# Optimization experiments

Hardware: AMD Instinct MI355X
Metric: run time of the kernel (lower is better)

The kernel has to match this reference:

```python
import jax, jax.numpy as jnp
import numpy as np

B, S, H, F, V, MAX_OOV = 128, 512, 1024, 512, 50000, 50


def setup_inputs() -> dict:
    key = jax.random.key(0)
    ks = jax.random.split(key, 20)
    r = lambda i, shp, s=0.02: (jax.random.normal(ks[i], shp, jnp.float32) * s)
    return dict(
        input=jax.random.randint(ks[0], (B,), 0, V),
        hidden=jax.random.normal(ks[1], (1, B, H), jnp.float32) * 0.1,
        encoder_outputs=jax.random.normal(ks[2], (B, S, H), jnp.float32) * 0.1,
        x_padding_masks=jnp.ones((B, S), jnp.float32),
        len_oov=jax.random.randint(ks[3], (B,), 0, MAX_OOV),
        coverage_vector=jnp.zeros((B, S), jnp.float32),
        ref2tgt=jax.random.randint(ks[4], (B, S), 0, V + MAX_OOV),
        emb=r(5, (V, F)),
        W_ih=r(6, (3 * H, F)), W_hh=r(7, (3 * H, H)),
        b_ih=jnp.zeros(3 * H, jnp.float32), b_hh=jnp.zeros(3 * H, jnp.float32),
        e2v1_w=r(8, (F, H)), e2v1_b=jnp.zeros(F, jnp.float32),
        e2v2_w=r(9, (V, F)), e2v2_b=jnp.zeros(V, jnp.float32),
        fc_w=r(10, (H, 2 * H)), fc_b=jnp.zeros(H, jnp.float32),
        wgen_w=r(11, (1, 2 * H + F)), wgen_b=jnp.zeros(1, jnp.float32),
        att_Wh=r(12, (H, H)), att_Ws=r(13, (H, H)),
        att_wc=r(14, (H,)), att_b=jnp.zeros(H, jnp.float32), att_v=r(15, (H,)),
    )


def reference(input, hidden, encoder_outputs, x_padding_masks, len_oov,
              coverage_vector, ref2tgt, emb, W_ih, W_hh, b_ih, b_hh,
              e2v1_w, e2v1_b, e2v2_w, e2v2_b, fc_w, fc_b, wgen_w, wgen_b,
              att_Wh, att_Ws, att_wc, att_b, att_v):
    # embedding lookup (dropout is identity at inference)
    emb_x = emb[input]  # [B, F]

    # --- additive (Bahdanau) attention with coverage ---
    s = hidden[0]  # [B, H] (n_layers == 1)
    feat = jnp.tanh(
        jnp.einsum('bsh,kh->bsk', encoder_outputs, att_Wh)
        + (s @ att_Ws.T)[:, None, :]
        + coverage_vector[:, :, None] * att_wc
        + att_b)  # [B, S, H]
    e = jnp.einsum('bsh,h->bs', feat, att_v)  # [B, S]
    a = jax.nn.softmax(e, axis=1) * x_padding_masks
    a = a / (jnp.sum(a, axis=1, keepdims=True))  # [B, S] renormalized attn
    coverage_new = coverage_vector + a
    context = jnp.einsum('bs,bsh->bh', a, encoder_outputs)  # [B, H]
    h_att = jnp.concatenate([s, context], axis=-1) @ fc_w.T + fc_b  # [B, H]

    # --- single-step GRU (PyTorch gate order r, z, n) ---
    gi = emb_x @ W_ih.T + b_ih  # [B, 3H]
    gh = h_att @ W_hh.T + b_hh  # [B, 3H]
    i_r, i_z, i_n = jnp.split(gi, 3, axis=-1)
    h_r, h_z, h_n = jnp.split(gh, 3, axis=-1)
    r = jax.nn.sigmoid(i_r + h_r)
    z = jax.nn.sigmoid(i_z + h_z)
    n = jnp.tanh(i_n + r * h_n)
    h_new = (1.0 - z) * n + z * h_att  # [B, H]

    # --- vocab distribution ---
    out1 = h_new @ e2v1_w.T + e2v1_b  # [B, F]
    p_vocab = jax.nn.softmax(out1 @ e2v2_w.T + e2v2_b, axis=1)  # [B, V]

    # --- pointer-generator mixing ---
    x_gen = jnp.concatenate([context, h_new, emb_x], axis=-1)  # [B, 2H+F]
    p_gen = jax.nn.sigmoid(x_gen @ wgen_w.T + wgen_b)[:, 0]  # [B]
    p_gen = jnp.clip(p_gen, 0.001, 0.999)
    p_vocab_w = p_gen[:, None] * p_vocab  # [B, V]
    attn_w = (1.0 - p_gen)[:, None] * a  # [B, S]
    p_ext = jnp.concatenate([p_vocab_w, jnp.zeros((B, MAX_OOV), p_vocab_w.dtype)], axis=1)
    rows = jnp.arange(B)[:, None]
    final = p_ext.at[rows, ref2tgt].add(attn_w)  # scatter_add over extended vocab

    return final, h_new[None], coverage_new, a
```

## Files before the change

### kernel.cpp

```cpp
#include <hip/hip_runtime.h>
#include <math.h>

#define B_   128
#define S_   512
#define H_   1024
#define F_   512
#define V_   50000
#define OOV_ 50
#define EV_  (V_ + OOV_)

#define BM 128
#define BN 128
#define BK 64

typedef __attribute__((ext_vector_type(8))) __bf16 bf16x8;
typedef __attribute__((ext_vector_type(4))) __bf16 bf16x4;
typedef __attribute__((ext_vector_type(4))) float  f32x4;

__device__ __forceinline__ void gload_lds16(const void* g, void* lds) {
  __builtin_amdgcn_global_load_lds(
      (const __attribute__((address_space(1))) unsigned int*)g,
      (__attribute__((address_space(3))) unsigned int*)lds, 16, 0, 0);
}

__device__ __forceinline__ float fast_tanh(float x) {
  float v = fminf(fmaxf(x, -15.f), 15.f);
  float t = __expf(2.f * v);
  return 1.f - 2.f / (t + 1.f);
}

__global__ __launch_bounds__(256)
void cast_both_kernel(const float* __restrict__ enc, __bf16* __restrict__ enc_h,
                      const float* __restrict__ wh, __bf16* __restrict__ wh_h)
{
  const size_t n_enc = (size_t)B_ * S_ * H_;
  const size_t n_tot = n_enc + (size_t)H_ * H_;
  for (size_t i = ((size_t)blockIdx.x * 256 + threadIdx.x) * 8; i < n_tot;
       i += (size_t)gridDim.x * 256 * 8) {
    const float* in; __bf16* out; size_t j;
    if (i < n_enc) { in = enc; out = enc_h; j = i; }
    else           { in = wh;  out = wh_h;  j = i - n_enc; }
    float4 a = *(const float4*)(in + j);
    float4 b = *(const float4*)(in + j + 4);
    bf16x8 o;
    o[0] = (__bf16)a.x; o[1] = (__bf16)a.y; o[2] = (__bf16)a.z; o[3] = (__bf16)a.w;
    o[4] = (__bf16)b.x; o[5] = (__bf16)b.y; o[6] = (__bf16)b.z; o[7] = (__bf16)b.w;
    *(bf16x8*)(out + j) = o;
  }
}

__global__ __launch_bounds__(256)
void gemm_splitk(const float* __restrict__ A, const float* __restrict__ W,
                 float* __restrict__ partial, int N, int K, int KS)
{
  __shared__ float As[128 * 68];
  __shared__ float Ws[32 * 68];
  const int tid = threadIdx.x;
  const int n0 = blockIdx.x * 32;
  const int p  = blockIdx.y;
  const int tx = tid & 7, ty = tid >> 3;
  const int lr = tid >> 4, lc4 = (tid & 15) * 4;
  float acc[4][4] = {};
  const int kend = p * KS + KS;
  for (int k0 = p * KS; k0 < kend; k0 += 64) {
#pragma unroll
    for (int pp = 0; pp < 8; ++pp)
      *(float4*)(As + (pp * 16 + lr) * 68 + lc4) =
          *(const float4*)(A + (size_t)(pp * 16 + lr) * K + k0 + lc4);
#pragma unroll
    for (int pp = 0; pp < 2; ++pp)
      *(float4*)(Ws + (pp * 16 + lr) * 68 + lc4) =
          *(const float4*)(W + (size_t)(n0 + pp * 16 + lr) * K + k0 + lc4);
    __syncthreads();
#pragma unroll
    for (int kk = 0; kk < 16; ++kk) {
      float4 av[4], wv[4];
#pragma unroll
      for (int i = 0; i < 4; i++) av[i] = *(const float4*)(As + (ty * 4 + i) * 68 + kk * 4);
#pragma unroll
      for (int j = 0; j < 4; j++) wv[j] = *(const float4*)(Ws + (tx * 4 + j) * 68 + kk * 4);
#pragma unroll
      for (int i = 0; i < 4; i++)
#pragma unroll
        for (int j = 0; j < 4; j++) {
          acc[i][j] = fmaf(av[i].x, wv[j].x, acc[i][j]);
          acc[i][j] = fmaf(av[i].y, wv[j].y, acc[i][j]);
          acc[i][j] = fmaf(av[i].z, wv[j].z, acc[i][j]);
          acc[i][j] = fmaf(av[i].w, wv[j].w, acc[i][j]);
        }
    }
    __syncthreads();
  }
#pragma unroll
  for (int i = 0; i < 4; i++)
#pragma unroll
    for (int j = 0; j < 4; j++)
      partial[((size_t)p * 128 + ty * 4 + i) * N + n0 + tx * 4 + j] = acc[i][j];
}

__global__ __launch_bounds__(256)
void gemm_splitk_cat(const float* __restrict__ A1, const float* __restrict__ A2,
                     const float* __restrict__ W, float* __restrict__ partial,
                     int N, int K, int KS)
{
  __shared__ float As[128 * 68];
  __shared__ float Ws[32 * 68];
  const int tid = threadIdx.x;
  const int n0 = blockIdx.x * 32;
  const int p  = blockIdx.y;
  const int tx = tid & 7, ty = tid >> 3;
  const int lr = tid >> 4, lc4 = (tid & 15) * 4;
  const float* A = (p * KS < 1024) ? A1 : A2;
  const int kbase = (p * KS < 1024) ? 0 : 1024;
  float acc[4][4] = {};
  const int kend = p * KS + KS;
  for (int k0 = p * KS; k0 < kend; k0 += 64) {
#pragma unroll
    for (int pp = 0; pp < 8; ++pp)
      *(float4*)(As + (pp * 16 + lr) * 68 + lc4) =
          *(const float4*)(A + (size_t)(pp * 16 + lr) * 1024 + (k0 - kbase) + lc4);
#pragma unroll
    for (int pp = 0; pp < 2; ++pp)
      *(float4*)(Ws + (pp * 16 + lr) * 68 + lc4) =
          *(const float4*)(W + (size_t)(n0 + pp * 16 + lr) * K + k0 + lc4);
    __syncthreads();
#pragma unroll
    for (int kk = 0; kk < 16; ++kk) {
      float4 av[4], wv[4];
#pragma unroll
      for (int i = 0; i < 4; i++) av[i] = *(const float4*)(As + (ty * 4 + i) * 68 + kk * 4);
#pragma unroll
      for (int j = 0; j < 4; j++) wv[j] = *(const float4*)(Ws + (tx * 4 + j) * 68 + kk * 4);
#pragma unroll
      for (int i = 0; i < 4; i++)
#pragma unroll
        for (int j = 0; j < 4; j++) {
          acc[i][j] = fmaf(av[i].x, wv[j].x, acc[i][j]);
          acc[i][j] = fmaf(av[i].y, wv[j].y, acc[i][j]);
          acc[i][j] = fmaf(av[i].z, wv[j].z, acc[i][j]);
          acc[i][j] = fmaf(av[i].w, wv[j].w, acc[i][j]);
        }
    }
    __syncthreads();
  }
#pragma unroll
  for (int i = 0; i < 4; i++)
#pragma unroll
    for (int j = 0; j < 4; j++)
      partial[((size_t)p * 128 + ty * 4 + i) * N + n0 + tx * 4 + j] = acc[i][j];
}

__global__ __launch_bounds__(256)
void gemm_splitk_gather(const int* __restrict__ input, const float* __restrict__ emb,
                        const float* __restrict__ W, float* __restrict__ partial,
                        int N, int K, int KS)
{
  __shared__ float As[128 * 68];
  __shared__ float Ws[32 * 68];
  const int tid = threadIdx.x;
  const int n0 = blockIdx.x * 32;
  const int p  = blockIdx.y;
  const int tx = tid & 7, ty = tid >> 3;
  const int lr = tid >> 4, lc4 = (tid & 15) * 4;
  float acc[4][4] = {};
  const int kend = p * KS + KS;
  for (int k0 = p * KS; k0 < kend; k0 += 64) {
#pragma unroll
    for (int pp = 0; pp < 8; ++pp) {
      int row = input[pp * 16 + lr];
      *(float4*)(As + (pp * 16 + lr) * 68 + lc4) =
          *(const float4*)(emb + (size_t)row * K + k0 + lc4);
    }
#pragma unroll
    for (int pp = 0; pp < 2; ++pp)
      *(float4*)(Ws + (pp * 16 + lr) * 68 + lc4) =
          *(const float4*)(W + (size_t)(n0 + pp * 16 + lr) * K + k0 + lc4);
    __syncthreads();
#pragma unroll
    for (int kk = 0; kk < 16; ++kk) {
      float4 av[4], wv[4];
#pragma unroll
      for (int i = 0; i < 4; i++) av[i] = *(const float4*)(As + (ty * 4 + i) * 68 + kk * 4);
#pragma unroll
      for (int j = 0; j < 4; j++) wv[j] = *(const float4*)(Ws + (tx * 4 + j) * 68 + kk * 4);
#pragma unroll
      for (int i = 0; i < 4; i++)
#pragma unroll
        for (int j = 0; j < 4; j++) {
          acc[i][j] = fmaf(av[i].x, wv[j].x, acc[i][j]);
          acc[i][j] = fmaf(av[i].y, wv[j].y, acc[i][j]);
          acc[i][j] = fmaf(av[i].z, wv[j].z, acc[i][j]);
          acc[i][j] = fmaf(av[i].w, wv[j].w, acc[i][j]);
        }
    }
    __syncthreads();
  }
#pragma unroll
  for (int i = 0; i < 4; i++)
#pragma unroll
    for (int j = 0; j < 4; j++)
      partial[((size_t)p * 128 + ty * 4 + i) * N + n0 + tx * 4 + j] = acc[i][j];
}

__global__ __launch_bounds__(256)
void reduce_partial(const float* __restrict__ partial, const float* __restrict__ bias,
                    float* __restrict__ C, int N, int P)
{
  int idx = blockIdx.x * 256 + threadIdx.x;
  int n = idx % N;
  float s = bias ? bias[n] : 0.f;
  for (int p = 0; p < P; ++p) s += partial[(size_t)p * 128 * N + idx];
  C[idx] = s;
}

__global__ __launch_bounds__(256)
void reduce_partial_bf16(const float* __restrict__ partial, const float* __restrict__ bias,
                         __bf16* __restrict__ C, int N, int P)
{
  int idx = blockIdx.x * 256 + threadIdx.x;
  int n = idx % N;
  float s = bias ? bias[n] : 0.f;
  for (int p = 0; p < P; ++p) s += partial[(size_t)p * 128 * N + idx];
  C[idx] = (__bf16)s;
}

__global__ __launch_bounds__(512, 1)
void feat_mfma256_kernel(const __bf16* __restrict__ enc, const __bf16* __restrict__ Wh,
                         const float* __restrict__ pSWS, const float* __restrict__ cov,
                         const float* __restrict__ wcv, const float* __restrict__ ab,
                         const float* __restrict__ av_, float* __restrict__ e_part)
{
  __shared__ __attribute__((aligned(16))) __bf16 As[2][2][128 * 64];
  __shared__ __attribute__((aligned(16))) __bf16 Bs[2][2][128 * 64];
  const int tid  = threadIdx.x;
  const int lane = tid & 63, wid = tid >> 6;
  const int wr = wid >> 2, wc = wid & 3;
  const int bid = blockIdx.x;
  const int swz = (bid & 7) * 128 + (bid >> 3);
  const int mt = swz >> 2, nt = swz & 3;
  const int bs0 = mt * 256;
  const int n0  = nt * 256;
  const int b   = bs0 >> 9;

  const int scb = ((tid & 7) * 16) ^ (((tid >> 3) & 7) << 4);
  const __bf16* aS[2][2];
  const __bf16* bS[2][2];
#pragma unroll
  for (int h = 0; h < 2; ++h)
#pragma unroll
    for (int q = 0; q < 2; ++q) {
      int r = h * 128 + q * 64 + (tid >> 3);
      aS[h][q] = enc + (size_t)(bs0 + r) * H_ + (scb >> 1);
      bS[h][q] = Wh  + (size_t)(n0  + r) * H_ + (scb >> 1);
    }
  const int ldsQ0 = tid * 16, ldsQ1 = 8192 + tid * 16;

  const int lrow = lane & 15, kbase = (lane >> 4) << 4;
  const int bh = wc >> 1;
  int aO[8][2], bO[4][2];
#pragma unroll
  for (int m = 0; m < 8; ++m) {
    int rh = m * 16 + lrow, sw = (rh & 7) << 4;
    aO[m][0] = rh * 128 + (kbase ^ sw);
    aO[m][1] = rh * 128 + ((64 + kbase) ^ sw);
  }
#pragma unroll
  for (int n = 0; n < 4; ++n) {
    int rh = (wc & 1) * 64 + n * 16 + lrow, sw = (rh & 7) << 4;
    bO[n][0] = rh * 128 + (kbase ^ sw);
    bO[n][1] = rh * 128 + ((64 + kbase) ^ sw);
  }

  f32x4 acc[8][4];
#pragma unroll
  for (int i = 0; i < 8; i++)
#pragma unroll
    for (int j = 0; j < 4; j++) acc[i][j] = (f32x4){0.f, 0.f, 0.f, 0.f};
  bf16x8 bfv[4][2];

#define STG_A(d, h, ofs)                                                       \
  { gload_lds16(aS[h][0] + (ofs), (char*)As[d][h] + ldsQ0);                    \
    gload_lds16(aS[h][1] + (ofs), (char*)As[d][h] + ldsQ1); }
#define STG_B(d, h, ofs)                                                       \
  { gload_lds16(bS[h][0] + (ofs), (char*)Bs[d][h] + ldsQ0);                    \
    gload_lds16(bS[h][1] + (ofs), (char*)Bs[d][h] + ldsQ1); }
#define BAR()                                                                  \
  { __builtin_amdgcn_sched_barrier(0); __builtin_amdgcn_s_barrier();           \
    __builtin_amdgcn_sched_barrier(0); }
#define LGKM0()                                                                \
  { asm volatile("s_waitcnt lgkmcnt(0)" ::: "memory");                         \
    __builtin_amdgcn_sched_barrier(0); }
#define VMC(n)                                                                 \
  { asm volatile("s_waitcnt vmcnt(" #n ")" ::: "memory");                      \
    __builtin_amdgcn_sched_barrier(0); }
#define RD_B(d)                                                                \
  { _Pragma("unroll")                                                          \
    for (int n = 0; n < 4; ++n) {                                              \
      bfv[n][0] = *(const bf16x8*)((const char*)Bs[d][bh] + bO[n][0]);         \
      bfv[n][1] = *(const bf16x8*)((const char*)Bs[d][bh] + bO[n][1]);         \
    } }
#define PH(d, q, STGSTMT, TAILWAIT)                                            \
  {                                                                            \
    bf16x8 x00 = *(const bf16x8*)((const char*)As[d][wr] + aO[2*(q)][0]);      \
    bf16x8 x01 = *(const bf16x8*)((const char*)As[d][wr] + aO[2*(q)][1]);      \
    bf16x8 x10 = *(const bf16x8*)((const char*)As[d][wr] + aO[2*(q)+1][0]);    \
    bf16x8 x11 = *(const bf16x8*)((const char*)As[d][wr] + aO[2*(q)+1][1]);    \
    STGSTMT;                                                                   \
    BAR(); LGKM0();                                                            \
    __builtin_amdgcn_s_setprio(1);                                             \
    _Pragma("unroll")                                                          \
    for (int n = 0; n < 4; ++n) {                                              \
      acc[2*(q)][n]   = __builtin_amdgcn_mfma_f32_16x16x32_bf16(x00, bfv[n][0], acc[2*(q)][n], 0, 0, 0);   \
      acc[2*(q)][n]   = __builtin_amdgcn_mfma_f32_16x16x32_bf16(x01, bfv[n][1], acc[2*(q)][n], 0, 0, 0);   \
      acc[2*(q)+1][n] = __builtin_amdgcn_mfma_f32_16x16x32_bf16(x10, bfv[n][0], acc[2*(q)+1][n], 0, 0, 0); \
      acc[2*(q)+1][n] = __builtin_amdgcn_mfma_f32_16x16x32_bf16(x11, bfv[n][1], acc[2*(q)+1][n], 0, 0, 0); \
    }                                                                          \
    __builtin_amdgcn_s_setprio(0);                                             \
    TAILWAIT; BAR();                                                           \
  }

  STG_B(0, 0, 0) STG_B(0, 1, 0) STG_A(0, 0, 0) STG_A(0, 1, 0)
  STG_B(1, 0, 64) STG_B(1, 1, 64)
  VMC(4); BAR();

#pragma unroll 1
  for (int i = 0; i < 7; ++i) {
    RD_B(0);
    PH(0, 0, STG_A(1, 0, 64), )
    PH(0, 1, STG_A(1, 1, 64), )
    PH(0, 2, STG_B(0, 0, 128), )
    PH(0, 3, STG_B(0, 1, 128), VMC(4))
    RD_B(1);
    PH(1, 0, STG_A(0, 0, 128), )
    PH(1, 1, STG_A(0, 1, 128), )
    PH(1, 2, STG_B(1, 0, 192), )
    PH(1, 3, STG_B(1, 1, 192), VMC(4))
#pragma unroll
    for (int h = 0; h < 2; ++h)
#pragma unroll
      for (int q = 0; q < 2; ++q) { aS[h][q] += 128; bS[h][q] += 128; }
  }
  RD_B(0);
  PH(0, 0, STG_A(1, 0, 64), )
  PH(0, 1, STG_A(1, 1, 64), )
  PH(0, 2, , )
  PH(0, 3, , VMC(0))
  RD_B(1);
  PH(1, 0, , )
  PH(1, 1, , )
  PH(1, 2, , )
  PH(1, 3, , )
  __syncthreads();
#undef STG_A
#undef STG_B
#undef BAR
#undef LGKM0
#undef VMC
#undef RD_B
#undef PH

  float rowsum[8][4];
#pragma unroll
  for (int m = 0; m < 8; m++)
#pragma unroll
    for (int j = 0; j < 4; j++) rowsum[m][j] = 0.f;

#pragma unroll
  for (int n = 0; n < 4; ++n) {
    int col_g = n0 + wc * 64 + n * 16 + (lane & 15);
    float sw = 0.f;
#pragma unroll
    for (int p = 0; p < 16; ++p) sw += pSWS[((size_t)p * 128 + b) * H_ + col_g];
    float wc_n = wcv[col_g], ab_n = ab[col_g], av_n = av_[col_g];
#pragma unroll
    for (int m = 0; m < 8; ++m) {
#pragma unroll
      for (int j = 0; j < 4; ++j) {
        int row_l = wr * 128 + m * 16 + ((lane >> 4) << 2) + j;
        float val = acc[m][n][j] + sw + cov[bs0 + row_l] * wc_n + ab_n;
        rowsum[m][j] += fast_tanh(val) * av_n;
      }
    }
  }
#pragma unroll
  for (int m = 0; m < 8; ++m)
#pragma unroll
    for (int j = 0; j < 4; ++j) {
      float v = rowsum[m][j];
      v += __shfl_xor(v, 1);
      v += __shfl_xor(v, 2);
      v += __shfl_xor(v, 4);
      v += __shfl_xor(v, 8);
      rowsum[m][j] = v;
    }
  float (*red)[4] = (float(*)[4])As;
  if ((lane & 15) == 0) {
#pragma unroll
    for (int m = 0; m < 8; ++m)
#pragma unroll
      for (int j = 0; j < 4; ++j)
        red[wr * 128 + m * 16 + ((lane >> 4) << 2) + j][wc] = rowsum[m][j];
  }
  __syncthreads();
  if (tid < 256)
    e_part[(size_t)nt * (B_ * S_) + bs0 + tid] =
        red[tid][0] + red[tid][1] + red[tid][2] + red[tid][3];
}

__global__ __launch_bounds__(256)
void logits_mfma_kernel(const __bf16* __restrict__ A, const float* __restrict__ W,
                        const float* __restrict__ bias, float* __restrict__ out0)
{
  __shared__ __attribute__((aligned(16))) __bf16 As[BM * BK];
  __shared__ __attribute__((aligned(16))) __bf16 Bs[BN * BK];
  const int tid  = threadIdx.x;
  const int lane = tid & 63, wid = tid >> 6;
  const int wr = wid >> 1, wcc = wid & 1;
  const int n0 = blockIdx.x * BN;

  f32x4 acc[4][4];
#pragma unroll
  for (int i = 0; i < 4; i++)
#pragma unroll
    for (int j = 0; j < 4; j++) acc[i][j] = (f32x4){0.f, 0.f, 0.f, 0.f};

  const float* wsrc[8];
  int wdst[8];
#pragma unroll
  for (int p = 0; p < 8; ++p) {
    int idx = p * 1024 + tid * 4;
    int r = idx >> 6, c = idx & 63;
    int row_g = n0 + r; if (row_g >= V_) row_g = V_ - 1;
    wsrc[p] = W + (size_t)row_g * F_ + c;
    wdst[p] = r * 128 + ((c * 2) ^ ((r & 7) << 4));
  }
  float4 wreg[8];
#pragma unroll
  for (int p = 0; p < 8; ++p) wreg[p] = *(const float4*)(wsrc[p]);

  for (int k0 = 0; k0 < F_; k0 += BK) {
#pragma unroll
    for (int p = 0; p < 4; ++p) {
      int off = p * 4096 + tid * 16;
      int r = off >> 7, cb = off & 127;
      int scb = cb ^ ((r & 7) << 4);
      gload_lds16(A + (size_t)r * F_ + k0 + (scb >> 1), (char*)As + off);
    }
#pragma unroll
    for (int p = 0; p < 8; ++p) {
      union { __bf16 h[4]; uint2 u; } t;
      t.h[0] = (__bf16)wreg[p].x; t.h[1] = (__bf16)wreg[p].y;
      t.h[2] = (__bf16)wreg[p].z; t.h[3] = (__bf16)wreg[p].w;
      *(uint2*)((char*)Bs + wdst[p]) = t.u;
    }
    __syncthreads();
    if (k0 + BK < F_) {
#pragma unroll
      for (int p = 0; p < 8; ++p) wreg[p] = *(const float4*)(wsrc[p] + k0 + BK);
    }

    bf16x8 af[4][2], bfv[4][2];
#pragma unroll
    for (int m = 0; m < 4; ++m) {
      int row = wr * 64 + m * 16 + (lane & 15);
      int swz = (row & 7) << 4;
#pragma unroll
      for (int kk = 0; kk < 2; ++kk) {
        int kb = kk * 64 + ((lane >> 4) << 4);
        af[m][kk] = *(const bf16x8*)((const char*)As + row * 128 + (kb ^ swz));
      }
    }
#pragma unroll
    for (int n = 0; n < 4; ++n) {
      int row = wcc * 64 + n * 16 + (lane & 15);
      int swz = (row & 7) << 4;
#pragma unroll
      for (int kk = 0; kk < 2; ++kk) {
        int kb = kk * 64 + ((lane >> 4) << 4);
        bfv[n][kk] = *(const bf16x8*)((const char*)Bs + row * 128 + (kb ^ swz));
      }
    }
#pragma unroll
    for (int m = 0; m < 4; ++m)
#pragma unroll
      for (int n = 0; n < 4; ++n)
#pragma unroll
        for (int kk = 0; kk < 2; ++kk)
          acc[m][n] = __builtin_amdgcn_mfma_f32_16x16x32_bf16(af[m][kk], bfv[n][kk], acc[m][n], 0, 0, 0);
    __syncthreads();
  }

#pragma unroll
  for (int m = 0; m < 4; ++m) {
#pragma unroll
    for (int n = 0; n < 4; ++n) {
      int col_g = n0 + wcc * 64 + n * 16 + (lane & 15);
      if (col_g >= V_) continue;
      float bv = bias[col_g];
#pragma unroll
      for (int j = 0; j < 4; ++j) {
        int row = wr * 64 + m * 16 + ((lane >> 4) << 2) + j;
        out0[(size_t)row * EV_ + col_g] = acc[m][n][j] + bv;
      }
    }
  }
}

__global__ __launch_bounds__(512)
void softmax_a_kernel(const float* __restrict__ e_part, const float* __restrict__ mask,
                      const float* __restrict__ cov, float* __restrict__ a_ws,
                      float* __restrict__ out_a, float* __restrict__ out_cov)
{
  const int b = blockIdx.x;
  const int s = threadIdx.x;
  __shared__ float red[512];
  float e = 0.f;
  for (int kt = 0; kt < 4; ++kt) e += e_part[(size_t)kt * (B_ * S_) + b * S_ + s];
  red[s] = e;
  __syncthreads();
  for (int st = 256; st > 0; st >>= 1) {
    if (s < st) red[s] = fmaxf(red[s], red[s + st]);
    __syncthreads();
  }
  float mx = red[0];
  __syncthreads();
  float ex = expf(e - mx) * mask[b * S_ + s];
  red[s] = ex;
  __syncthreads();
  for (int st = 256; st > 0; st >>= 1) {
    if (s < st) red[s] += red[s + st];
    __syncthreads();
  }
  float a = ex / red[0];
  a_ws[b * S_ + s] = a;
  out_a[b * S_ + s] = a;
  out_cov[b * S_ + s] = cov[b * S_ + s] + a;
}

__global__ __launch_bounds__(256)
void context_kernel(const float* __restrict__ a_ws, const __bf16* __restrict__ enc,
                    float* __restrict__ ctx)
{
  const int b = blockIdx.y, q = blockIdx.x;
  const int lane = threadIdx.x & 63, w = threadIdx.x >> 6;
  const int h0 = q * 256 + lane * 4;
  __shared__ float al[S_];
  __shared__ float part[4][256];
  for (int i = threadIdx.x; i < S_; i += 256) al[i] = a_ws[b * S_ + i];
  __syncthreads();
  float acc0 = 0.f, acc1 = 0.f, acc2 = 0.f, acc3 = 0.f;
  const __bf16* ep = enc + (size_t)b * S_ * H_ + h0;
#pragma unroll 4
  for (int s = w * 128; s < w * 128 + 128; ++s) {
    bf16x4 v = *(const bf16x4*)(ep + (size_t)s * H_);
    float a = al[s];
    acc0 = fmaf(a, (float)v[0], acc0);
    acc1 = fmaf(a, (float)v[1], acc1);
    acc2 = fmaf(a, (float)v[2], acc2);
    acc3 = fmaf(a, (float)v[3], acc3);
  }
  part[w][lane * 4 + 0] = acc0;
  part[w][lane * 4 + 1] = acc1;
  part[w][lane * 4 + 2] = acc2;
  part[w][lane * 4 + 3] = acc3;
  __syncthreads();
  if (threadIdx.x < 256) {
    int o = threadIdx.x;
    ctx[b * H_ + q * 256 + o] = part[0][o] + part[1][o] + part[2][o] + part[3][o];
  }
}

__global__ __launch_bounds__(256)
void gru_kernel(const float* __restrict__ pgi, const float* __restrict__ pgh,
                const float* __restrict__ b_ih, const float* __restrict__ b_hh,
                const float* __restrict__ h_att, float* __restrict__ h_new_ws,
                float* __restrict__ out_h)
{
  int idx = blockIdx.x * 256 + threadIdx.x;
  int b = idx >> 10, h = idx & 1023;
  float ir = b_ih[h], iz = b_ih[H_ + h], in_ = b_ih[2 * H_ + h];
  float hr = b_hh[h], hz = b_hh[H_ + h], hn = b_hh[2 * H_ + h];
#pragma unroll
  for (int p = 0; p < 8; ++p) {
    const float* gp = pgi + (size_t)p * 128 * 3072 + (size_t)b * 3072;
    ir += gp[h]; iz += gp[H_ + h]; in_ += gp[2 * H_ + h];
    const float* hp = pgh + (size_t)p * 128 * 3072 + (size_t)b * 3072;
    hr += hp[h]; hz += hp[H_ + h]; hn += hp[2 * H_ + h];
  }
  float r = 1.f / (1.f + expf(-(ir + hr)));
  float z = 1.f / (1.f + expf(-(iz + hz)));
  float n = tanhf(in_ + r * hn);
  float ha = h_att[(size_t)b * H_ + h];
  float hv = (1.f - z) * n + z * ha;
  h_new_ws[idx] = hv;
  out_h[idx] = hv;
}

__global__ __launch_bounds__(512)
void stats_pgen_kernel(const float* __restrict__ logits, float* __restrict__ vmax,
                       float* __restrict__ vsum, const float* __restrict__ context,
                       const float* __restrict__ h_new, const int* __restrict__ input,
                       const float* __restrict__ emb, const float* __restrict__ wgen_w,
                       const float* __restrict__ wgen_b, float* __restrict__ pgen)
{
  __shared__ float red[512];
  if (blockIdx.x < B_) {
    int b = blockIdx.x;
    const float* row = logits + (size_t)b * EV_;
    float m = -1e30f;
    for (int v = threadIdx.x * 2; v < V_; v += 1024) {
      float2 x = *(const float2*)(row + v);
      m = fmaxf(m, fmaxf(x.x, x.y));
    }
    red[threadIdx.x] = m;
    __syncthreads();
    for (int st = 256; st > 0; st >>= 1) {
      if (threadIdx.x < st) red[threadIdx.x] = fmaxf(red[threadIdx.x], red[threadIdx.x + st]);
      __syncthreads();
    }
    m = red[0];
    __syncthreads();
    float ssum = 0.f;
    for (int v = threadIdx.x * 2; v < V_; v += 1024) {
      float2 x = *(const float2*)(row + v);
      ssum += expf(x.x - m) + expf(x.y - m);
    }
    red[threadIdx.x] = ssum;
    __syncthreads();
    for (int st = 256; st > 0; st >>= 1) {
      if (threadIdx.x < st) red[threadIdx.x] += red[threadIdx.x + st];
      __syncthreads();
    }
    if (threadIdx.x == 0) { vmax[b] = m; vsum[b] = red[0]; }
  } else {
    int b = blockIdx.x - B_;
    const float* erow = emb + (size_t)input[b] * F_;
    float acc = 0.f;
    for (int j = threadIdx.x; j < H_; j += 512) acc = fmaf(context[b * H_ + j], wgen_w[j], acc);
    for (int j = threadIdx.x; j < H_; j += 512) acc = fmaf(h_new[b * H_ + j], wgen_w[H_ + j], acc);
    for (int j = threadIdx.x; j < F_; j += 512) acc = fmaf(erow[j], wgen_w[2 * H_ + j], acc);
    red[threadIdx.x] = acc;
    __syncthreads();
    for (int st = 256; st > 0; st >>= 1) {
      if (threadIdx.x < st) red[threadIdx.x] += red[threadIdx.x + st];
      __syncthreads();
    }
    if (threadIdx.x == 0) {
      float p = 1.f / (1.f + expf(-(red[0] + wgen_b[0])));
      p = fminf(fmaxf(p, 0.001f), 0.999f);
      pgen[b] = p;
    }
  }
}

__global__ void final_kernel(float* __restrict__ out0, const float* __restrict__ vmax,
                             const float* __restrict__ vsum, const float* __restrict__ pgen)
{
  int b = blockIdx.y;
  int v = blockIdx.x * 256 + threadIdx.x;
  if (v >= EV_) return;
  float* row = out0 + (size_t)b * EV_;
  if (v < V_) row[v] = pgen[b] * expf(row[v] - vmax[b]) / vsum[b];
  else row[v] = 0.f;
}

__global__ void scatter_kernel(const int* __restrict__ ref2tgt, const float* __restrict__ a_ws,
                               const float* __restrict__ pgen, float* __restrict__ out0)
{
  int b = blockIdx.x;
  int s = threadIdx.x;
  float w = (1.f - pgen[b]) * a_ws[b * S_ + s];
  int t = ref2tgt[b * S_ + s];
  atomicAdd(&out0[(size_t)b * EV_ + t], w);
}

extern "C" void kernel_launch(void* const* d_in, const int* in_sizes, int n_in,
                              void* d_out, int out_size, void* d_ws, size_t ws_size,
                              hipStream_t stream)
{
  const int*   input   = (const int*)d_in[0];
  const float* hidden  = (const float*)d_in[1];
  const float* enc     = (const float*)d_in[2];
  const float* mask    = (const float*)d_in[3];
  const float* cov     = (const float*)d_in[5];
  const int*   ref2tgt = (const int*)d_in[6];
  const float* emb     = (const float*)d_in[7];
  const float* W_ih    = (const float*)d_in[8];
  const float* W_hh    = (const float*)d_in[9];
  const float* b_ih    = (const float*)d_in[10];
  const float* b_hh    = (const float*)d_in[11];
  const float* e2v1_w  = (const float*)d_in[12];
  const float* e2v1_b  = (const float*)d_in[13];
  const float* e2v2_w  = (const float*)d_in[14];
  const float* e2v2_b  = (const float*)d_in[15];
  const float* fc_w    = (const float*)d_in[16];
  const float* fc_b    = (const float*)d_in[17];
  const float* wgen_w  = (const float*)d_in[18];
  const float* wgen_b  = (const float*)d_in[19];
  const float* att_Wh  = (const float*)d_in[20];
  const float* att_Ws  = (const float*)d_in[21];
  const float* att_wc  = (const float*)d_in[22];
  const float* att_b   = (const float*)d_in[23];
  const float* att_v   = (const float*)d_in[24];

  char* w = (char*)d_ws;
  __bf16* enc_h  = (__bf16*)w;  w += (size_t)B_ * S_ * H_ * 2;
  __bf16* Wh_h   = (__bf16*)w;  w += (size_t)H_ * H_ * 2;
  __bf16* out1_h = (__bf16*)w;  w += (size_t)B_ * F_ * 2;
  float* e_part  = (float*)w;   w += (size_t)4 * B_ * S_ * 4;
  float* a_ws    = (float*)w;   w += (size_t)B_ * S_ * 4;
  float* context = (float*)w;   w += (size_t)B_ * H_ * 4;
  float* h_att   = (float*)w;   w += (size_t)B_ * H_ * 4;
  float* h_new   = (float*)w;   w += (size_t)B_ * H_ * 4;
  float* pgen    = (float*)w;   w += 128 * 4;
  float* vmax    = (float*)w;   w += 128 * 4;
  float* vsum    = (float*)w;   w += 128 * 4;
  float* pA      = (float*)w;   w += (size_t)16 * 128 * 1024 * 4;
  float* pB      = (float*)w;   w += (size_t)8 * 128 * 3072 * 4;
  float* pC      = (float*)w;   w += (size_t)8 * 128 * 3072 * 4;

  float* out0    = (float*)d_out;
  float* out_h   = out0 + (size_t)B_ * EV_;
  float* out_cov = out_h + (size_t)B_ * H_;
  float* out_a   = out_cov + (size_t)B_ * S_;

  cast_both_kernel<<<4096, 256, 0, stream>>>(enc, enc_h, att_Wh, Wh_h);
  gemm_splitk<<<dim3(32, 16), 256, 0, stream>>>(hidden, att_Ws, pA, H_, H_, 64);
  feat_mfma256_kernel<<<dim3(1024), 512, 0, stream>>>(enc_h, Wh_h, pA, cov, att_wc, att_b, att_v, e_part);
  softmax_a_kernel<<<B_, 512, 0, stream>>>(e_part, mask, cov, a_ws, out_a, out_cov);
  context_kernel<<<dim3(4, B_), 256, 0, stream>>>(a_ws, enc_h, context);
  gemm_splitk_cat<<<dim3(32, 16), 256, 0, stream>>>(hidden, context, fc_w, pA, H_, 2 * H_, 128);
  reduce_partial<<<512, 256, 0, stream>>>(pA, fc_b, h_att, H_, 16);
  gemm_splitk_gather<<<dim3(96, 8), 256, 0, stream>>>(input, emb, W_ih, pB, 3 * H_, F_, 64);
  gemm_splitk<<<dim3(96, 8), 256, 0, stream>>>(h_att, W_hh, pC, 3 * H_, H_, 128);
  gru_kernel<<<(B_ * H_) / 256, 256, 0, stream>>>(pB, pC, b_ih, b_hh, h_att, h_new, out_h);
  gemm_splitk<<<dim3(16, 16), 256, 0, stream>>>(h_new, e2v1_w, pA, F_, H_, 64);
  reduce_partial_bf16<<<256, 256, 0, stream>>>(pA, e2v1_b, out1_h, F_, 16);
  logits_mfma_kernel<<<dim3((V_ + BN - 1) / BN), 256, 0, stream>>>(out1_h, e2v2_w, e2v2_b, out0);
  stats_pgen_kernel<<<2 * B_, 512, 0, stream>>>(out0, vmax, vsum, context, h_new, input, emb,
                                                wgen_w, wgen_b, pgen);
  final_kernel<<<dim3((EV_ + 255) / 256, B_), 256, 0, stream>>>(out0, vmax, vsum, pgen);
  scatter_kernel<<<B_, 512, 0, stream>>>(ref2tgt, a_ws, pgen, out0);
}
```

Baseline: 448.4 us.

## Fuse encoder fp32-to-bf16 cast into attention GEMM A-tile staging

Drops the separate pass that converted the 256 MB fp32 encoder tensor to bf16. The feat GEMM now loads fp32 rows into registers, converts them and writes swizzled bf16 into LDS inside its pipeline. The context kernel reads the fp32 encoder directly. This removes a full read plus write of the encoder, but uses more registers and VGPR traffic in the GEMM, and the context kernel now reads twice the bytes.

Result: slower. 519.8 us (+15.9%).

```diff
diff --git a/kernel.cpp b/kernel.cpp
--- a/kernel.cpp
+++ b/kernel.cpp
@@ -30,23 +30,15 @@
 }
 
 __global__ __launch_bounds__(256)
-void cast_both_kernel(const float* __restrict__ enc, __bf16* __restrict__ enc_h,
-                      const float* __restrict__ wh, __bf16* __restrict__ wh_h)
-{
-  const size_t n_enc = (size_t)B_ * S_ * H_;
-  const size_t n_tot = n_enc + (size_t)H_ * H_;
-  for (size_t i = ((size_t)blockIdx.x * 256 + threadIdx.x) * 8; i < n_tot;
-       i += (size_t)gridDim.x * 256 * 8) {
-    const float* in; __bf16* out; size_t j;
-    if (i < n_enc) { in = enc; out = enc_h; j = i; }
-    else           { in = wh;  out = wh_h;  j = i - n_enc; }
-    float4 a = *(const float4*)(in + j);
-    float4 b = *(const float4*)(in + j + 4);
-    bf16x8 o;
-    o[0] = (__bf16)a.x; o[1] = (__bf16)a.y; o[2] = (__bf16)a.z; o[3] = (__bf16)a.w;
-    o[4] = (__bf16)b.x; o[5] = (__bf16)b.y; o[6] = (__bf16)b.z; o[7] = (__bf16)b.w;
-    *(bf16x8*)(out + j) = o;
-  }
+void cast_wh_kernel(const float* __restrict__ wh, __bf16* __restrict__ wh_h)
+{
+  size_t i = ((size_t)blockIdx.x * 256 + threadIdx.x) * 8;
+  float4 a = *(const float4*)(wh + i);
+  float4 b = *(const float4*)(wh + i + 4);
+  bf16x8 o;
+  o[0] = (__bf16)a.x; o[1] = (__bf16)a.y; o[2] = (__bf16)a.z; o[3] = (__bf16)a.w;
+  o[4] = (__bf16)b.x; o[5] = (__bf16)b.y; o[6] = (__bf16)b.z; o[7] = (__bf16)b.w;
+  *(bf16x8*)(wh_h + i) = o;
 }
 
 __global__ __launch_bounds__(256)
@@ -225,7 +217,7 @@
 }
 
 __global__ __launch_bounds__(512, 1)
-void feat_mfma256_kernel(const __bf16* __restrict__ enc, const __bf16* __restrict__ Wh,
+void feat_mfma256_kernel(const float* __restrict__ enc, const __bf16* __restrict__ Wh,
                          const float* __restrict__ pSWS, const float* __restrict__ cov,
                          const float* __restrict__ wcv, const float* __restrict__ ab,
                          const float* __restrict__ av_, float* __restrict__ e_part)
@@ -243,17 +235,22 @@
   const int b   = bs0 >> 9;
 
   const int scb = ((tid & 7) * 16) ^ (((tid >> 3) & 7) << 4);
-  const __bf16* aS[2][2];
   const __bf16* bS[2][2];
 #pragma unroll
   for (int h = 0; h < 2; ++h)
 #pragma unroll
     for (int q = 0; q < 2; ++q) {
       int r = h * 128 + q * 64 + (tid >> 3);
-      aS[h][q] = enc + (size_t)(bs0 + r) * H_ + (scb >> 1);
-      bS[h][q] = Wh  + (size_t)(n0  + r) * H_ + (scb >> 1);
+      bS[h][q] = Wh + (size_t)(n0 + r) * H_ + (scb >> 1);
     }
   const int ldsQ0 = tid * 16, ldsQ1 = 8192 + tid * 16;
+
+  const float* aF00 = enc + (size_t)(bs0 +   0 + (tid >> 3)) * H_ + (tid & 7) * 8;
+  const float* aF01 = enc + (size_t)(bs0 +  64 + (tid >> 3)) * H_ + (tid & 7) * 8;
+  const float* aF10 = enc + (size_t)(bs0 + 128 + (tid >> 3)) * H_ + (tid & 7) * 8;
+  const float* aF11 = enc + (size_t)(bs0 + 192 + (tid >> 3)) * H_ + (tid & 7) * 8;
+  const int wOfs = ((tid >> 3) * 128) + (((tid & 7) * 16) ^ (((tid >> 3) & 7) << 4));
+  float4 sA[8], sB[8];
 
   const int lrow = lane & 15, kbase = (lane >> 4) << 4;
   const int bh = wc >> 1;
@@ -278,9 +275,24 @@
     for (int j = 0; j < 4; j++) acc[i][j] = (f32x4){0.f, 0.f, 0.f, 0.f};
   bf16x8 bfv[4][2];
 
-#define STG_A(d, h, ofs)                                                       \
-  { gload_lds16(aS[h][0] + (ofs), (char*)As[d][h] + ldsQ0);                    \
-    gload_lds16(aS[h][1] + (ofs), (char*)As[d][h] + ldsQ1); }
+#define LA_H0(S, ofs)                                                          \
+  { S[0] = *(const float4*)(aF00 + (ofs)); S[1] = *(const float4*)(aF00 + (ofs) + 4); \
+    S[2] = *(const float4*)(aF01 + (ofs)); S[3] = *(const float4*)(aF01 + (ofs) + 4); }
+#define LA_H1(S, ofs)                                                          \
+  { S[4] = *(const float4*)(aF10 + (ofs)); S[5] = *(const float4*)(aF10 + (ofs) + 4); \
+    S[6] = *(const float4*)(aF11 + (ofs)); S[7] = *(const float4*)(aF11 + (ofs) + 4); }
+#define WA_H(d, h, S)                                                          \
+  { bf16x8 o0, o1;                                                             \
+    o0[0] = (__bf16)S[(h)*4+0].x; o0[1] = (__bf16)S[(h)*4+0].y;                \
+    o0[2] = (__bf16)S[(h)*4+0].z; o0[3] = (__bf16)S[(h)*4+0].w;                \
+    o0[4] = (__bf16)S[(h)*4+1].x; o0[5] = (__bf16)S[(h)*4+1].y;                \
+    o0[6] = (__bf16)S[(h)*4+1].z; o0[7] = (__bf16)S[(h)*4+1].w;                \
+    o1[0] = (__bf16)S[(h)*4+2].x; o1[1] = (__bf16)S[(h)*4+2].y;                \
+    o1[2] = (__bf16)S[(h)*4+2].z; o1[3] = (__bf16)S[(h)*4+2].w;                \
+    o1[4] = (__bf16)S[(h)*4+3].x; o1[5] = (__bf16)S[(h)*4+3].y;                \
+    o1[6] = (__bf16)S[(h)*4+3].z; o1[7] = (__bf16)S[(h)*4+3].w;                \
+    *(bf16x8*)((char*)As[d][h] + wOfs) = o0;                                   \
+    *(bf16x8*)((char*)As[d][h] + wOfs + 8192) = o1; }
 #define STG_B(d, h, ofs)                                                       \
   { gload_lds16(bS[h][0] + (ofs), (char*)Bs[d][h] + ldsQ0);                    \
     gload_lds16(bS[h][1] + (ofs), (char*)Bs[d][h] + ldsQ1); }
@@ -319,30 +331,35 @@
     TAILWAIT; BAR();                                                           \
   }
 
-  STG_B(0, 0, 0) STG_B(0, 1, 0) STG_A(0, 0, 0) STG_A(0, 1, 0)
+  STG_B(0, 0, 0) STG_B(0, 1, 0)
   STG_B(1, 0, 64) STG_B(1, 1, 64)
-  VMC(4); BAR();
+  LA_H0(sA, 0) LA_H1(sA, 0)
+  WA_H(0, 0, sA) WA_H(0, 1, sA)
+  LA_H0(sB, 64) LA_H1(sB, 64)
+  VMC(12);
+  LGKM0(); BAR();
 
 #pragma unroll 1
   for (int i = 0; i < 7; ++i) {
     RD_B(0);
-    PH(0, 0, STG_A(1, 0, 64), )
-    PH(0, 1, STG_A(1, 1, 64), )
+    PH(0, 0, { LA_H0(sA, 128); WA_H(1, 0, sB); }, )
+    PH(0, 1, { LA_H1(sA, 128); WA_H(1, 1, sB); }, )
     PH(0, 2, STG_B(0, 0, 128), )
-    PH(0, 3, STG_B(0, 1, 128), VMC(4))
+    PH(0, 3, STG_B(0, 1, 128), VMC(12))
     RD_B(1);
-    PH(1, 0, STG_A(0, 0, 128), )
-    PH(1, 1, STG_A(0, 1, 128), )
+    PH(1, 0, { LA_H0(sB, 192); WA_H(0, 0, sA); }, )
+    PH(1, 1, { LA_H1(sB, 192); WA_H(0, 1, sA); }, )
     PH(1, 2, STG_B(1, 0, 192), )
-    PH(1, 3, STG_B(1, 1, 192), VMC(4))
+    PH(1, 3, STG_B(1, 1, 192), VMC(12))
+    aF00 += 128; aF01 += 128; aF10 += 128; aF11 += 128;
 #pragma unroll
     for (int h = 0; h < 2; ++h)
 #pragma unroll
-      for (int q = 0; q < 2; ++q) { aS[h][q] += 128; bS[h][q] += 128; }
+      for (int q = 0; q < 2; ++q) bS[h][q] += 128;
   }
   RD_B(0);
-  PH(0, 0, STG_A(1, 0, 64), )
-  PH(0, 1, STG_A(1, 1, 64), )
+  PH(0, 0, WA_H(1, 0, sB), )
+  PH(0, 1, WA_H(1, 1, sB), )
   PH(0, 2, , )
   PH(0, 3, , VMC(0))
   RD_B(1);
@@ -351,7 +368,9 @@
   PH(1, 2, , )
   PH(1, 3, , )
   __syncthreads();
-#undef STG_A
+#undef LA_H0
+#undef LA_H1
+#undef WA_H
 #undef STG_B
 #undef BAR
 #undef LGKM0
@@ -443,8 +462,8 @@
     for (int p = 0; p < 4; ++p) {
       int off = p * 4096 + tid * 16;
       int r = off >> 7, cb = off & 127;
-      int scb = cb ^ ((r & 7) << 4);
-      gload_lds16(A + (size_t)r * F_ + k0 + (scb >> 1), (char*)As + off);
+      int scb2 = cb ^ ((r & 7) << 4);
+      gload_lds16(A + (size_t)r * F_ + k0 + (scb2 >> 1), (char*)As + off);
     }
 #pragma unroll
     for (int p = 0; p < 8; ++p) {
@@ -538,7 +557,7 @@
 }
 
 __global__ __launch_bounds__(256)
-void context_kernel(const float* __restrict__ a_ws, const __bf16* __restrict__ enc,
+void context_kernel(const float* __restrict__ a_ws, const float* __restrict__ enc,
                     float* __restrict__ ctx)
 {
   const int b = blockIdx.y, q = blockIdx.x;
@@ -549,15 +568,15 @@
   for (int i = threadIdx.x; i < S_; i += 256) al[i] = a_ws[b * S_ + i];
   __syncthreads();
   float acc0 = 0.f, acc1 = 0.f, acc2 = 0.f, acc3 = 0.f;
-  const __bf16* ep = enc + (size_t)b * S_ * H_ + h0;
+  const float* ep = enc + (size_t)b * S_ * H_ + h0;
 #pragma unroll 4
   for (int s = w * 128; s < w * 128 + 128; ++s) {
-    bf16x4 v = *(const bf16x4*)(ep + (size_t)s * H_);
+    float4 v = *(const float4*)(ep + (size_t)s * H_);
     float a = al[s];
-    acc0 = fmaf(a, (float)v[0], acc0);
-    acc1 = fmaf(a, (float)v[1], acc1);
-    acc2 = fmaf(a, (float)v[2], acc2);
-    acc3 = fmaf(a, (float)v[3], acc3);
+    acc0 = fmaf(a, v.x, acc0);
+    acc1 = fmaf(a, v.y, acc1);
+    acc2 = fmaf(a, v.z, acc2);
+    acc3 = fmaf(a, v.w, acc3);
   }
   part[w][lane * 4 + 0] = acc0;
   part[w][lane * 4 + 1] = acc1;
@@ -704,7 +723,6 @@
   const float* att_v   = (const float*)d_in[24];
 
   char* w = (char*)d_ws;
-  __bf16* enc_h  = (__bf16*)w;  w += (size_t)B_ * S_ * H_ * 2;
   __bf16* Wh_h   = (__bf16*)w;  w += (size_t)H_ * H_ * 2;
   __bf16* out1_h = (__bf16*)w;  w += (size_t)B_ * F_ * 2;
   float* e_part  = (float*)w;   w += (size_t)4 * B_ * S_ * 4;
@@ -724,11 +742,11 @@
   float* out_cov = out_h + (size_t)B_ * H_;
   float* out_a   = out_cov + (size_t)B_ * S_;
 
-  cast_both_kernel<<<4096, 256, 0, stream>>>(enc, enc_h, att_Wh, Wh_h);
+  cast_wh_kernel<<<512, 256, 0, stream>>>(att_Wh, Wh_h);
   gemm_splitk<<<dim3(32, 16), 256, 0, stream>>>(hidden, att_Ws, pA, H_, H_, 64);
-  feat_mfma256_kernel<<<dim3(1024), 512, 0, stream>>>(enc_h, Wh_h, pA, cov, att_wc, att_b, att_v, e_part);
+  feat_mfma256_kernel<<<dim3(1024), 512, 0, stream>>>(enc, Wh_h, pA, cov, att_wc, att_b, att_v, e_part);
   softmax_a_kernel<<<B_, 512, 0, stream>>>(e_part, mask, cov, a_ws, out_a, out_cov);
-  context_kernel<<<dim3(4, B_), 256, 0, stream>>>(a_ws, enc_h, context);
+  context_kernel<<<dim3(4, B_), 256, 0, stream>>>(a_ws, enc, context);
   gemm_splitk_cat<<<dim3(32, 16), 256, 0, stream>>>(hidden, context, fc_w, pA, H_, 2 * H_, 128);
   reduce_partial<<<512, 256, 0, stream>>>(pA, fc_b, h_att, H_, 16);
   gemm_splitk_gather<<<dim3(96, 8), 256, 0, stream>>>(input, emb, W_ih, pB, 3 * H_, F_, 64);
```
